# Optimization experiments

Hardware: AMD Instinct MI355X
Metric: run time of the kernel (lower is better)

Reference implementation:

```python
import jax, jax.numpy as jnp
import numpy as np

N = 50000      # nodes
E = 800000     # edges
IN_DIM = 128
HID = 64
OUT = 2


def _sage_conv(h, src, dst, Wl, bl, Wr, n_nodes):
    """PyG SAGEConv (mean aggr): lin_l(mean_{j in N(i)} h_j) + lin_r(h_i).
    Messages flow src -> dst. lin_r has no bias (PyG default)."""
    msg = h[src]                                             # [E, d]
    agg = jax.ops.segment_sum(msg, dst, num_segments=n_nodes)  # [N, d]
    cnt = jax.ops.segment_sum(jnp.ones((msg.shape[0],), h.dtype), dst,
                              num_segments=n_nodes)          # [N]
    agg = agg / jnp.maximum(cnt, 1.0)[:, None]               # mean, zero-deg safe
    return agg @ Wl + bl + h @ Wr


def setup_inputs() -> dict:
    key = jax.random.key(0)
    ks = jax.random.split(key, 12)
    def lin(k, fan_in, fan_out):
        s = 1.0 / np.sqrt(fan_in)
        return jax.random.uniform(k, (fan_in, fan_out), jnp.float32, -s, s)
    x = jax.random.normal(ks[0], (N, IN_DIM), jnp.float32)
    edge_index = jax.random.randint(ks[1], (2, E), 0, N, jnp.int64)
    return {
        "x": x,
        "edge_index": edge_index,
        # conv1
        "W1l": lin(ks[2], IN_DIM, HID),
        "b1l": jnp.zeros((HID,), jnp.float32),
        "W1r": lin(ks[3], IN_DIM, HID),
        # conv2
        "W2l": lin(ks[4], HID, HID),
        "b2l": jnp.zeros((HID,), jnp.float32),
        "W2r": lin(ks[5], HID, HID),
        # edge MLP
        "Wm1": lin(ks[6], 2 * HID, HID),
        "bm1": jnp.zeros((HID,), jnp.float32),
        "Wm2": lin(ks[7], HID, OUT),
        "bm2": jnp.zeros((OUT,), jnp.float32),
    }


def reference(x, edge_index, W1l, b1l, W1r, W2l, b2l, W2r, Wm1, bm1, Wm2, bm2):
    src, dst = edge_index[0], edge_index[1]
    h = jax.nn.relu(_sage_conv(x, src, dst, W1l, b1l, W1r, N))   # [N, HID]
    h = jax.nn.relu(_sage_conv(h, src, dst, W2l, b2l, W2r, N))   # [N, HID]
    edge_rep = jnp.concatenate([h[src], h[dst]], axis=1)          # [E, 2*HID]
    hidden = jax.nn.relu(edge_rep @ Wm1 + bm1)                    # [E, HID]
    return hidden @ Wm2 + bm2                                     # [E, OUT]
```

## Files before the change

kernel.cpp:

```cpp
#include <hip/hip_runtime.h>

#define N_NODES 50000
#define N_EDGES 800000

#define BVALS 64
#define NBUK ((N_NODES + BVALS - 1) / BVALS)
#define PAD 16
#define CHUNK 4096
#define NSB ((N_EDGES + CHUNK - 1) / CHUNK)
#define BCAP 2048
#define PREPB 128

typedef __attribute__((ext_vector_type(8))) short bf16x8;
typedef __attribute__((ext_vector_type(4))) float f32x4;


__device__ __forceinline__ float bf2f(unsigned short u) {
    return __uint_as_float(((unsigned)u) << 16);
}
__device__ __forceinline__ unsigned short f2bf(float f) {
    unsigned u = __float_as_uint(f);
    u += 0x7FFFu + ((u >> 16) & 1u);
    return (unsigned short)(u >> 16);
}
__device__ __forceinline__ unsigned pack2bf(float a, float b) {
    return (unsigned)f2bf(a) | ((unsigned)f2bf(b) << 16);
}
__device__ __forceinline__ float lobf(int w) {
    return __uint_as_float(((unsigned)w) << 16);
}
__device__ __forceinline__ float hibf(int w) {
    return __uint_as_float(((unsigned)w) & 0xFFFF0000u);
}
__device__ __forceinline__ void stv(float* p, float v) { *p = v; }
__device__ __forceinline__ void stv(unsigned short* p, float v) { *p = f2bf(v); }

__device__ __forceinline__ void add8(float* a, int4 v) {
    a[0] += lobf(v.x); a[1] += hibf(v.x);
    a[2] += lobf(v.y); a[3] += hibf(v.y);
    a[4] += lobf(v.z); a[5] += hibf(v.z);
    a[6] += lobf(v.w); a[7] += hibf(v.w);
}


__global__ __launch_bounds__(256) void count_prep_kernel(
        const int* __restrict__ ei, int* __restrict__ bhist,
        const float* __restrict__ W1l, const float* __restrict__ W1r,
        const float* __restrict__ W2l, const float* __restrict__ W2r,
        const float* __restrict__ Wm1,
        unsigned short* __restrict__ wt1, unsigned short* __restrict__ wt2,
        unsigned short* __restrict__ wtm, int E) {
    __shared__ int hist[NBUK];
    int t = threadIdx.x;
    if (blockIdx.x >= NSB) {
        int id = (blockIdx.x - NSB) * 256 + t;
        if (id < 128 * 128) {
            int k = id >> 7, c = id & 127;
            float v = (c < 64) ? W1l[k * 64 + c] : W1r[k * 64 + (c - 64)];
            wt1[c * 128 + k] = f2bf(v);
        } else if (id < 128 * 128 + 64 * 128) {
            int j = id - 128 * 128;
            int k = j >> 7, c = j & 127;
            float v = (c < 64) ? W2l[k * 64 + c] : W2r[k * 64 + (c - 64)];
            wt2[c * 64 + k] = f2bf(v);
        } else if (id < 128 * 128 + 64 * 128 + 64 * 128) {
            int j = id - 128 * 128 - 64 * 128;
            int k = j >> 7, c = j & 127;
            float v = (c < 64) ? Wm1[k * 64 + c] : Wm1[(64 + k) * 64 + (c - 64)];
            wtm[c * 64 + k] = f2bf(v);
        }
        return;
    }
    for (int h = t; h < NBUK; h += 256) hist[h] = 0;
    __syncthreads();
    int e0 = blockIdx.x * CHUNK;
    int ne = min(CHUNK, E - e0);
    for (int i = t; i < ne; i += 256)
        atomicAdd(&hist[ei[E + e0 + i] >> 6], 1);
    __syncthreads();
    for (int h = t; h < NBUK; h += 256)
        bhist[blockIdx.x * NBUK + h] = hist[h];
}

__global__ __launch_bounds__(1024) void scan_bcnt_kernel(
        const int* __restrict__ bhist, int* __restrict__ bofs,
        int* __restrict__ gcur_pad) {
    __shared__ int lds[1024];
    int t = threadIdx.x;
    int v = 0;
    if (t < NBUK)
        for (int b = 0; b < NSB; ++b) v += bhist[b * NBUK + t];
    lds[t] = v;
    __syncthreads();
    for (int off = 1; off < 1024; off <<= 1) {
        int u = (t >= off) ? lds[t - off] : 0;
        __syncthreads();
        lds[t] += u;
        __syncthreads();
    }
    if (t <= NBUK) bofs[t] = lds[t] - ((t < NBUK) ? v : 0);
    if (t < NBUK) gcur_pad[t * PAD] = lds[t] - v;
}

__global__ __launch_bounds__(256) void scatter_kernel(
        const int* __restrict__ ei, int* __restrict__ gcur_pad,
        unsigned int* __restrict__ bpk, int E) {
    __shared__ unsigned int pk[CHUNK];
    __shared__ int hist[NBUK];
    __shared__ int lbase[NBUK];
    int t = threadIdx.x;
    for (int h = t; h < NBUK; h += 256) hist[h] = 0;
    __syncthreads();
    int e0 = blockIdx.x * CHUNK;
    int ne = min(CHUNK, E - e0);
    for (int i = t; i < ne; i += 256) {
        unsigned s = (unsigned)ei[e0 + i];
        unsigned d = (unsigned)ei[E + e0 + i];
        pk[i] = (d << 16) | s;
        atomicAdd(&hist[d >> 6], 1);
    }
    __syncthreads();
    for (int h = t; h < NBUK; h += 256) {
        int c = hist[h];
        lbase[h] = c ? atomicAdd(&gcur_pad[h * PAD], c) : 0;
        hist[h] = 0;
    }
    __syncthreads();
    for (int i = t; i < ne; i += 256) {
        unsigned v = pk[i];
        int h = (v >> 16) >> 6;
        int idx = atomicAdd(&hist[h], 1);
        bpk[lbase[h] + idx] = v;
    }
}


template<int K>
__device__ __forceinline__ void stage_w(
        const unsigned short* __restrict__ WT, unsigned short* w_lds, int t) {
    constexpr int KP = K + 8;
    for (int idx = t; idx < 128 * K / 8; idx += 256) {
        int f = idx * 8;
        int r = f / K, c = f % K;
        *(int4*)&w_lds[r * KP + c] = *(const int4*)&WT[r * K + c];
    }
}

template<int K, typename T0, typename T1>
__device__ __forceinline__ void mfma_tile(
        const unsigned short* a_lds, const unsigned short* w_lds,
        int t, int n0, T0* __restrict__ C0, T1* __restrict__ C1, int N) {
    constexpr int KP = K + 8;
    int w = t >> 6, l = t & 63;
    int lr = l & 15;
    int lk = (l >> 4) * 8;

    f32x4 acc[8];
#pragma unroll
    for (int i = 0; i < 8; ++i) acc[i] = (f32x4)(0.f);

#pragma unroll
    for (int kc = 0; kc < K / 32; ++kc) {
        bf16x8 af = *(const bf16x8*)&a_lds[(w * 16 + lr) * KP + kc * 32 + lk];
#pragma unroll
        for (int ct = 0; ct < 8; ++ct) {
            bf16x8 bfr = *(const bf16x8*)&w_lds[(ct * 16 + lr) * KP + kc * 32 + lk];
            acc[ct] = __builtin_amdgcn_mfma_f32_16x16x32_bf16(af, bfr, acc[ct], 0, 0, 0);
        }
    }

    int orow = n0 + w * 16 + (l >> 4) * 4;
#pragma unroll
    for (int ct = 0; ct < 4; ++ct) {
#pragma unroll
        for (int r = 0; r < 4; ++r) {
            if (orow + r < N) stv(&C0[(size_t)(orow + r) * 64 + ct * 16 + lr], acc[ct][r]);
        }
    }
#pragma unroll
    for (int ct = 4; ct < 8; ++ct) {
#pragma unroll
        for (int r = 0; r < 4; ++r) {
            if (orow + r < N) stv(&C1[(size_t)(orow + r) * 64 + (ct - 4) * 16 + lr], acc[ct][r]);
        }
    }
}


__global__ __launch_bounds__(256) void sort_gemm1_kernel(
        const unsigned int* __restrict__ bpk, const int* __restrict__ bofs,
        int* __restrict__ rowptr, int* __restrict__ elist,
        const float* __restrict__ x, const unsigned short* __restrict__ wt1,
        unsigned short* __restrict__ C0, float* __restrict__ C1, int N) {
    __shared__ __align__(16) char smem[52224];
    int t = threadIdx.x;

    if (blockIdx.x < NBUK) {
        unsigned int* pk = (unsigned int*)smem;
        int* sc  = (int*)(pk + BCAP);
        int* cur = sc + BVALS;
        int b = blockIdx.x;
        int e0 = bofs[b];
        int nb = min(bofs[b + 1] - e0, BCAP);

        if (t < BVALS) sc[t] = 0;
        __syncthreads();
        for (int i = t; i < nb; i += 256) {
            unsigned v = bpk[e0 + i];
            pk[i] = v;
            atomicAdd(&sc[(v >> 16) & 63], 1);
        }
        __syncthreads();
        int hv = (t < BVALS) ? sc[t] : 0;
#pragma unroll
        for (int off = 1; off < BVALS; off <<= 1) {
            int u = (t < BVALS && t >= off) ? sc[t - off] : 0;
            __syncthreads();
            if (t < BVALS) sc[t] += u;
            __syncthreads();
        }
        if (t < BVALS) {
            int ex = sc[t] - hv;
            cur[t] = ex;
            int n = b * BVALS + t;
            if (n <= N) rowptr[n] = e0 + ex;
        }
        __syncthreads();
        for (int i = t; i < nb; i += 256) {
            unsigned v = pk[i];
            int pos = atomicAdd(&cur[(v >> 16) & 63], 1);
            elist[e0 + pos] = v & 0xFFFF;
        }
        return;
    }

    constexpr int K = 128, KP = K + 8;
    unsigned short* a_lds = (unsigned short*)smem;
    unsigned short* w_lds = a_lds + 64 * KP;
    int n0 = (blockIdx.x - NBUK) * 64;

    for (int idx = t; idx < 64 * K / 4; idx += 256) {
        int f = idx * 4;
        int r = f / K, c = f % K;
        float4 v = make_float4(0.f, 0.f, 0.f, 0.f);
        if (n0 + r < N) v = *(const float4*)&x[(size_t)(n0 + r) * K + c];
        ushort4 o;
        o.x = f2bf(v.x); o.y = f2bf(v.y); o.z = f2bf(v.z); o.w = f2bf(v.w);
        *(ushort4*)&a_lds[r * KP + c] = o;
    }
    stage_w<K>(wt1, w_lds, t);
    __syncthreads();
    mfma_tile<K>(a_lds, w_lds, t, n0, C0, C1, N);
}


template<typename T1>
__global__ __launch_bounds__(256) void agg_gemm_kernel(
        const unsigned short* __restrict__ P, const float* __restrict__ R,
        const float* __restrict__ bias,
        const int* __restrict__ rowptr, const int* __restrict__ elist,
        const unsigned short* __restrict__ WT,
        unsigned short* __restrict__ C0, T1* __restrict__ C1, int N) {
    constexpr int K = 64, KP = K + 8;
    __shared__ unsigned short a_lds[64 * KP];
    __shared__ unsigned short w_lds[128 * KP];
    int t = threadIdx.x;
    int n0 = blockIdx.x * 64;

    stage_w<K>(WT, w_lds, t);

    int l8 = t & 7;
    int nr = t >> 3;
    float4 b0 = *(const float4*)&bias[l8 * 8];
    float4 b1 = *(const float4*)&bias[l8 * 8 + 4];

#pragma unroll
    for (int half = 0; half < 2; ++half) {
        int r = half * 32 + nr;
        int n = n0 + r;
        float a0[8] = {0.f, 0.f, 0.f, 0.f, 0.f, 0.f, 0.f, 0.f};
        float a1[8] = {0.f, 0.f, 0.f, 0.f, 0.f, 0.f, 0.f, 0.f};
        int r0 = 0, r1 = 0;
        if (n < N) { r0 = rowptr[n]; r1 = rowptr[n + 1]; }
        int p = r0;
        for (; p + 2 <= r1; p += 2) {
            int sA = elist[p], sB = elist[p + 1];
            int4 vA = *(const int4*)&P[(size_t)sA * 64 + l8 * 8];
            int4 vB = *(const int4*)&P[(size_t)sB * 64 + l8 * 8];
            add8(a0, vA);
            add8(a1, vB);
        }
        if (p < r1) {
            int sA = elist[p];
            add8(a0, *(const int4*)&P[(size_t)sA * 64 + l8 * 8]);
        }
        int4 o = make_int4(0, 0, 0, 0);
        if (n < N) {
            float inv = 1.0f / fmaxf((float)(r1 - r0), 1.0f);
            float4 rA = *(const float4*)&R[(size_t)n * 64 + l8 * 8];
            float4 rB = *(const float4*)&R[(size_t)n * 64 + l8 * 8 + 4];
            float h0 = fmaxf(fmaf(a0[0] + a1[0], inv, b0.x + rA.x), 0.f);
            float h1 = fmaxf(fmaf(a0[1] + a1[1], inv, b0.y + rA.y), 0.f);
            float h2 = fmaxf(fmaf(a0[2] + a1[2], inv, b0.z + rA.z), 0.f);
            float h3 = fmaxf(fmaf(a0[3] + a1[3], inv, b0.w + rA.w), 0.f);
            float h4 = fmaxf(fmaf(a0[4] + a1[4], inv, b1.x + rB.x), 0.f);
            float h5 = fmaxf(fmaf(a0[5] + a1[5], inv, b1.y + rB.y), 0.f);
            float h6 = fmaxf(fmaf(a0[6] + a1[6], inv, b1.z + rB.z), 0.f);
            float h7 = fmaxf(fmaf(a0[7] + a1[7], inv, b1.w + rB.w), 0.f);
            o.x = pack2bf(h0, h1); o.y = pack2bf(h2, h3);
            o.z = pack2bf(h4, h5); o.w = pack2bf(h6, h7);
        }
        *(int4*)&a_lds[r * KP + l8 * 8] = o;
    }
    __syncthreads();
    mfma_tile<K>(a_lds, w_lds, t, n0, C0, C1, N);
}


__global__ __launch_bounds__(256) void edge_out_kernel(
        const unsigned short* __restrict__ Pa, const unsigned short* __restrict__ Pb,
        const int* __restrict__ ei,
        const float* __restrict__ bm1,
        const float* __restrict__ Wm2, const float* __restrict__ bm2,
        float* __restrict__ out, int E) {
    int t = threadIdx.x;
    int l8 = t & 7;
    int eg = t >> 3;
    int base = blockIdx.x * 128 + eg;

    float4 wA = *(const float4*)&Wm2[l8 * 16];
    float4 wB = *(const float4*)&Wm2[l8 * 16 + 4];
    float4 wC = *(const float4*)&Wm2[l8 * 16 + 8];
    float4 wD = *(const float4*)&Wm2[l8 * 16 + 12];
    float4 bbA = *(const float4*)&bm1[l8 * 8];
    float4 bbB = *(const float4*)&bm1[l8 * 8 + 4];
    float ob0 = bm2[0], ob1 = bm2[1];

#pragma unroll
    for (int it = 0; it < 4; ++it) {
        int e = base + it * 32;
        int s = ei[e];
        int d = ei[E + e];
        int4 ua = *(const int4*)&Pa[(size_t)s * 64 + l8 * 8];
        int4 ub = *(const int4*)&Pb[(size_t)d * 64 + l8 * 8];
        float h0 = fmaxf(lobf(ua.x) + lobf(ub.x) + bbA.x, 0.f);
        float h1 = fmaxf(hibf(ua.x) + hibf(ub.x) + bbA.y, 0.f);
        float h2 = fmaxf(lobf(ua.y) + lobf(ub.y) + bbA.z, 0.f);
        float h3 = fmaxf(hibf(ua.y) + hibf(ub.y) + bbA.w, 0.f);
        float h4 = fmaxf(lobf(ua.z) + lobf(ub.z) + bbB.x, 0.f);
        float h5 = fmaxf(hibf(ua.z) + hibf(ub.z) + bbB.y, 0.f);
        float h6 = fmaxf(lobf(ua.w) + lobf(ub.w) + bbB.z, 0.f);
        float h7 = fmaxf(hibf(ua.w) + hibf(ub.w) + bbB.w, 0.f);
        float s0 = h0 * wA.x + h1 * wA.z + h2 * wB.x + h3 * wB.z
                 + h4 * wC.x + h5 * wC.z + h6 * wD.x + h7 * wD.z;
        float s1 = h0 * wA.y + h1 * wA.w + h2 * wB.y + h3 * wB.w
                 + h4 * wC.y + h5 * wC.w + h6 * wD.y + h7 * wD.w;
#pragma unroll
        for (int off = 4; off >= 1; off >>= 1) {
            s0 += __shfl_xor(s0, off, 64);
            s1 += __shfl_xor(s1, off, 64);
        }
        if (l8 == 0) {
            *(float2*)&out[(size_t)e * 2] = make_float2(s0 + ob0, s1 + ob1);
        }
    }
}


extern "C" void kernel_launch(void* const* d_in, const int* in_sizes, int n_in,
                              void* d_out, int out_size, void* d_ws, size_t ws_size,
                              hipStream_t stream) {
    const float* x   = (const float*)d_in[0];
    const int*   ei  = (const int*)d_in[1];
    const float* W1l = (const float*)d_in[2];
    const float* b1l = (const float*)d_in[3];
    const float* W1r = (const float*)d_in[4];
    const float* W2l = (const float*)d_in[5];
    const float* b2l = (const float*)d_in[6];
    const float* W2r = (const float*)d_in[7];
    const float* Wm1 = (const float*)d_in[8];
    const float* bm1 = (const float*)d_in[9];
    const float* Wm2 = (const float*)d_in[10];
    const float* bm2 = (const float*)d_in[11];
    float* out = (float*)d_out;

    const int N = N_NODES, E = N_EDGES;

    float* B0 = (float*)d_ws;
    float* B1 = B0 + (size_t)N * 64;
    float* B2 = B1 + (size_t)N * 64;
    unsigned short* B3h = (unsigned short*)(B2 + (size_t)N * 64);
    int* rowptr   = (int*)(B3h + (size_t)N * 64);
    int* elist    = rowptr + N + 1;
    int* bofs     = elist + E;
    int* gcur_pad = bofs + NBUK + 1;
    int* bhist    = gcur_pad + NBUK * PAD;
    unsigned short* wt1 = (unsigned short*)(bhist + NSB * NBUK);
    unsigned short* wt2 = wt1 + 128 * 128;
    unsigned short* wtm = wt2 + 128 * 64;
    unsigned int* bpk = (unsigned int*)B2;

    unsigned short* B0h = (unsigned short*)B0;
    unsigned short* B2h = (unsigned short*)B2;

    count_prep_kernel<<<NSB + PREPB, 256, 0, stream>>>(
        ei, bhist, W1l, W1r, W2l, W2r, Wm1, wt1, wt2, wtm, E);
    scan_bcnt_kernel<<<1, 1024, 0, stream>>>(bhist, bofs, gcur_pad);
    scatter_kernel<<<NSB, 256, 0, stream>>>(ei, gcur_pad, bpk, E);

    sort_gemm1_kernel<<<NBUK + (N + 63) / 64, 256, 0, stream>>>(
        bpk, bofs, rowptr, elist, x, wt1, B0h, B1, N);

    agg_gemm_kernel<float><<<(N + 63) / 64, 256, 0, stream>>>(
        B0h, B1, b1l, rowptr, elist, wt2, B2h, B1, N);

    agg_gemm_kernel<unsigned short><<<(N + 63) / 64, 256, 0, stream>>>(
        B2h, B1, b2l, rowptr, elist, wtm, B0h, B3h, N);

    edge_out_kernel<<<E / 128, 256, 0, stream>>>(B0h, B3h, ei, bm1, Wm2, bm2, out, E);
}
```

Measured before the change: 142.2 us.

## Process edge MLP per destination node via CSR and store root term in bf16

The sort now carries each edge's original index, so the edge-output kernel can walk the CSR per destination node. It loads the destination projection and bias once per node and scatters results to the original edge positions. It also stores the lin_r/root intermediate as bf16 instead of fp32 and unrolls the aggregation loop to four accumulators. Costs: the sort traffic doubles (uint2 entries), an extra eidx array is written and read, output writes become scattered, and load balance depends on node degree.

After: 165.5 us, median of 2. 1.16x slower.

```diff
diff --git a/kernel.cpp b/kernel.cpp
--- a/kernel.cpp
+++ b/kernel.cpp
@@ -102,10 +102,11 @@
     if (t < NBUK) gcur_pad[t * PAD] = lds[t] - v;
 }
 
+
 __global__ __launch_bounds__(256) void scatter_kernel(
         const int* __restrict__ ei, int* __restrict__ gcur_pad,
-        unsigned int* __restrict__ bpk, int E) {
-    __shared__ unsigned int pk[CHUNK];
+        uint2* __restrict__ bpk, int E) {
+    __shared__ uint2 pk[CHUNK];
     __shared__ int hist[NBUK];
     __shared__ int lbase[NBUK];
     int t = threadIdx.x;
@@ -116,7 +117,7 @@
     for (int i = t; i < ne; i += 256) {
         unsigned s = (unsigned)ei[e0 + i];
         unsigned d = (unsigned)ei[E + e0 + i];
-        pk[i] = (d << 16) | s;
+        pk[i] = make_uint2((d << 16) | s, (unsigned)(e0 + i));
         atomicAdd(&hist[d >> 6], 1);
     }
     __syncthreads();
@@ -127,8 +128,8 @@
     }
     __syncthreads();
     for (int i = t; i < ne; i += 256) {
-        unsigned v = pk[i];
-        int h = (v >> 16) >> 6;
+        uint2 v = pk[i];
+        int h = (v.x >> 16) >> 6;
         int idx = atomicAdd(&hist[h], 1);
         bpk[lbase[h] + idx] = v;
     }
@@ -188,15 +189,15 @@
 
 
 __global__ __launch_bounds__(256) void sort_gemm1_kernel(
-        const unsigned int* __restrict__ bpk, const int* __restrict__ bofs,
-        int* __restrict__ rowptr, int* __restrict__ elist,
+        const uint2* __restrict__ bpk, const int* __restrict__ bofs,
+        int* __restrict__ rowptr, int* __restrict__ elist, int* __restrict__ eidx,
         const float* __restrict__ x, const unsigned short* __restrict__ wt1,
-        unsigned short* __restrict__ C0, float* __restrict__ C1, int N) {
+        unsigned short* __restrict__ C0, unsigned short* __restrict__ C1, int N) {
     __shared__ __align__(16) char smem[52224];
     int t = threadIdx.x;
 
     if (blockIdx.x < NBUK) {
-        unsigned int* pk = (unsigned int*)smem;
+        uint2* pk = (uint2*)smem;
         int* sc  = (int*)(pk + BCAP);
         int* cur = sc + BVALS;
         int b = blockIdx.x;
@@ -206,9 +207,9 @@
         if (t < BVALS) sc[t] = 0;
         __syncthreads();
         for (int i = t; i < nb; i += 256) {
-            unsigned v = bpk[e0 + i];
+            uint2 v = bpk[e0 + i];
             pk[i] = v;
-            atomicAdd(&sc[(v >> 16) & 63], 1);
+            atomicAdd(&sc[(v.x >> 16) & 63], 1);
         }
         __syncthreads();
         int hv = (t < BVALS) ? sc[t] : 0;
@@ -227,9 +228,10 @@
         }
         __syncthreads();
         for (int i = t; i < nb; i += 256) {
-            unsigned v = pk[i];
-            int pos = atomicAdd(&cur[(v >> 16) & 63], 1);
-            elist[e0 + pos] = v & 0xFFFF;
+            uint2 v = pk[i];
+            int pos = e0 + atomicAdd(&cur[(v.x >> 16) & 63], 1);
+            elist[pos] = v.x & 0xFFFF;
+            eidx[pos] = (int)v.y;
         }
         return;
     }
@@ -254,13 +256,12 @@
 }
 
 
-template<typename T1>
 __global__ __launch_bounds__(256) void agg_gemm_kernel(
-        const unsigned short* __restrict__ P, const float* __restrict__ R,
+        const unsigned short* __restrict__ P, const unsigned short* __restrict__ R,
         const float* __restrict__ bias,
         const int* __restrict__ rowptr, const int* __restrict__ elist,
         const unsigned short* __restrict__ WT,
-        unsigned short* __restrict__ C0, T1* __restrict__ C1, int N) {
+        unsigned short* __restrict__ C0, unsigned short* __restrict__ C1, int N) {
     constexpr int K = 64, KP = K + 8;
     __shared__ unsigned short a_lds[64 * KP];
     __shared__ unsigned short w_lds[128 * KP];
@@ -280,33 +281,36 @@
         int n = n0 + r;
         float a0[8] = {0.f, 0.f, 0.f, 0.f, 0.f, 0.f, 0.f, 0.f};
         float a1[8] = {0.f, 0.f, 0.f, 0.f, 0.f, 0.f, 0.f, 0.f};
+        float a2[8] = {0.f, 0.f, 0.f, 0.f, 0.f, 0.f, 0.f, 0.f};
+        float a3[8] = {0.f, 0.f, 0.f, 0.f, 0.f, 0.f, 0.f, 0.f};
         int r0 = 0, r1 = 0;
         if (n < N) { r0 = rowptr[n]; r1 = rowptr[n + 1]; }
         int p = r0;
-        for (; p + 2 <= r1; p += 2) {
-            int sA = elist[p], sB = elist[p + 1];
+        for (; p + 4 <= r1; p += 4) {
+            int sA = elist[p],     sB = elist[p + 1];
+            int sC = elist[p + 2], sD = elist[p + 3];
             int4 vA = *(const int4*)&P[(size_t)sA * 64 + l8 * 8];
             int4 vB = *(const int4*)&P[(size_t)sB * 64 + l8 * 8];
-            add8(a0, vA);
-            add8(a1, vB);
-        }
-        if (p < r1) {
+            int4 vC = *(const int4*)&P[(size_t)sC * 64 + l8 * 8];
+            int4 vD = *(const int4*)&P[(size_t)sD * 64 + l8 * 8];
+            add8(a0, vA); add8(a1, vB); add8(a2, vC); add8(a3, vD);
+        }
+        for (; p < r1; ++p) {
             int sA = elist[p];
             add8(a0, *(const int4*)&P[(size_t)sA * 64 + l8 * 8]);
         }
         int4 o = make_int4(0, 0, 0, 0);
         if (n < N) {
             float inv = 1.0f / fmaxf((float)(r1 - r0), 1.0f);
-            float4 rA = *(const float4*)&R[(size_t)n * 64 + l8 * 8];
-            float4 rB = *(const float4*)&R[(size_t)n * 64 + l8 * 8 + 4];
-            float h0 = fmaxf(fmaf(a0[0] + a1[0], inv, b0.x + rA.x), 0.f);
-            float h1 = fmaxf(fmaf(a0[1] + a1[1], inv, b0.y + rA.y), 0.f);
-            float h2 = fmaxf(fmaf(a0[2] + a1[2], inv, b0.z + rA.z), 0.f);
-            float h3 = fmaxf(fmaf(a0[3] + a1[3], inv, b0.w + rA.w), 0.f);
-            float h4 = fmaxf(fmaf(a0[4] + a1[4], inv, b1.x + rB.x), 0.f);
-            float h5 = fmaxf(fmaf(a0[5] + a1[5], inv, b1.y + rB.y), 0.f);
-            float h6 = fmaxf(fmaf(a0[6] + a1[6], inv, b1.z + rB.z), 0.f);
-            float h7 = fmaxf(fmaf(a0[7] + a1[7], inv, b1.w + rB.w), 0.f);
+            int4 rv = *(const int4*)&R[(size_t)n * 64 + l8 * 8];
+            float h0 = fmaxf(fmaf(a0[0] + a1[0] + a2[0] + a3[0], inv, b0.x + lobf(rv.x)), 0.f);
+            float h1 = fmaxf(fmaf(a0[1] + a1[1] + a2[1] + a3[1], inv, b0.y + hibf(rv.x)), 0.f);
+            float h2 = fmaxf(fmaf(a0[2] + a1[2] + a2[2] + a3[2], inv, b0.z + lobf(rv.y)), 0.f);
+            float h3 = fmaxf(fmaf(a0[3] + a1[3] + a2[3] + a3[3], inv, b0.w + hibf(rv.y)), 0.f);
+            float h4 = fmaxf(fmaf(a0[4] + a1[4] + a2[4] + a3[4], inv, b1.x + lobf(rv.z)), 0.f);
+            float h5 = fmaxf(fmaf(a0[5] + a1[5] + a2[5] + a3[5], inv, b1.y + hibf(rv.z)), 0.f);
+            float h6 = fmaxf(fmaf(a0[6] + a1[6] + a2[6] + a3[6], inv, b1.z + lobf(rv.w)), 0.f);
+            float h7 = fmaxf(fmaf(a0[7] + a1[7] + a2[7] + a3[7], inv, b1.w + hibf(rv.w)), 0.f);
             o.x = pack2bf(h0, h1); o.y = pack2bf(h2, h3);
             o.z = pack2bf(h4, h5); o.w = pack2bf(h6, h7);
         }
@@ -319,14 +323,15 @@
 
 __global__ __launch_bounds__(256) void edge_out_kernel(
         const unsigned short* __restrict__ Pa, const unsigned short* __restrict__ Pb,
-        const int* __restrict__ ei,
+        const int* __restrict__ rowptr, const int* __restrict__ elist,
+        const int* __restrict__ eidx,
         const float* __restrict__ bm1,
         const float* __restrict__ Wm2, const float* __restrict__ bm2,
-        float* __restrict__ out, int E) {
+        float* __restrict__ out, int N) {
     int t = threadIdx.x;
     int l8 = t & 7;
-    int eg = t >> 3;
-    int base = blockIdx.x * 128 + eg;
+    int n = blockIdx.x * 32 + (t >> 3);
+    if (n >= N) return;
 
     float4 wA = *(const float4*)&Wm2[l8 * 16];
     float4 wB = *(const float4*)&Wm2[l8 * 16 + 4];
@@ -336,21 +341,57 @@
     float4 bbB = *(const float4*)&bm1[l8 * 8 + 4];
     float ob0 = bm2[0], ob1 = bm2[1];
 
-#pragma unroll
-    for (int it = 0; it < 4; ++it) {
-        int e = base + it * 32;
-        int s = ei[e];
-        int d = ei[E + e];
-        int4 ua = *(const int4*)&Pa[(size_t)s * 64 + l8 * 8];
-        int4 ub = *(const int4*)&Pb[(size_t)d * 64 + l8 * 8];
-        float h0 = fmaxf(lobf(ua.x) + lobf(ub.x) + bbA.x, 0.f);
-        float h1 = fmaxf(hibf(ua.x) + hibf(ub.x) + bbA.y, 0.f);
-        float h2 = fmaxf(lobf(ua.y) + lobf(ub.y) + bbA.z, 0.f);
-        float h3 = fmaxf(hibf(ua.y) + hibf(ub.y) + bbA.w, 0.f);
-        float h4 = fmaxf(lobf(ua.z) + lobf(ub.z) + bbB.x, 0.f);
-        float h5 = fmaxf(hibf(ua.z) + hibf(ub.z) + bbB.y, 0.f);
-        float h6 = fmaxf(lobf(ua.w) + lobf(ub.w) + bbB.z, 0.f);
-        float h7 = fmaxf(hibf(ua.w) + hibf(ub.w) + bbB.w, 0.f);
+    int4 vb = *(const int4*)&Pb[(size_t)n * 64 + l8 * 8];
+    float q0 = lobf(vb.x) + bbA.x, q1 = hibf(vb.x) + bbA.y;
+    float q2 = lobf(vb.y) + bbA.z, q3 = hibf(vb.y) + bbA.w;
+    float q4 = lobf(vb.z) + bbB.x, q5 = hibf(vb.z) + bbB.y;
+    float q6 = lobf(vb.w) + bbB.z, q7 = hibf(vb.w) + bbB.w;
+
+    int r0 = rowptr[n], r1 = rowptr[n + 1];
+    int p = r0;
+    for (; p + 2 <= r1; p += 2) {
+        int sA = elist[p], sB = elist[p + 1];
+        int4 ua = *(const int4*)&Pa[(size_t)sA * 64 + l8 * 8];
+        int4 ub = *(const int4*)&Pa[(size_t)sB * 64 + l8 * 8];
+        float h0 = fmaxf(lobf(ua.x) + q0, 0.f), g0 = fmaxf(lobf(ub.x) + q0, 0.f);
+        float h1 = fmaxf(hibf(ua.x) + q1, 0.f), g1 = fmaxf(hibf(ub.x) + q1, 0.f);
+        float h2 = fmaxf(lobf(ua.y) + q2, 0.f), g2 = fmaxf(lobf(ub.y) + q2, 0.f);
+        float h3 = fmaxf(hibf(ua.y) + q3, 0.f), g3 = fmaxf(hibf(ub.y) + q3, 0.f);
+        float h4 = fmaxf(lobf(ua.z) + q4, 0.f), g4 = fmaxf(lobf(ub.z) + q4, 0.f);
+        float h5 = fmaxf(hibf(ua.z) + q5, 0.f), g5 = fmaxf(hibf(ub.z) + q5, 0.f);
+        float h6 = fmaxf(lobf(ua.w) + q6, 0.f), g6 = fmaxf(lobf(ub.w) + q6, 0.f);
+        float h7 = fmaxf(hibf(ua.w) + q7, 0.f), g7 = fmaxf(hibf(ub.w) + q7, 0.f);
+        float sa0 = h0 * wA.x + h1 * wA.z + h2 * wB.x + h3 * wB.z
+                  + h4 * wC.x + h5 * wC.z + h6 * wD.x + h7 * wD.z;
+        float sa1 = h0 * wA.y + h1 * wA.w + h2 * wB.y + h3 * wB.w
+                  + h4 * wC.y + h5 * wC.w + h6 * wD.y + h7 * wD.w;
+        float sb0 = g0 * wA.x + g1 * wA.z + g2 * wB.x + g3 * wB.z
+                  + g4 * wC.x + g5 * wC.z + g6 * wD.x + g7 * wD.z;
+        float sb1 = g0 * wA.y + g1 * wA.w + g2 * wB.y + g3 * wB.w
+                  + g4 * wC.y + g5 * wC.w + g6 * wD.y + g7 * wD.w;
+#pragma unroll
+        for (int off = 4; off >= 1; off >>= 1) {
+            sa0 += __shfl_xor(sa0, off, 64);
+            sa1 += __shfl_xor(sa1, off, 64);
+            sb0 += __shfl_xor(sb0, off, 64);
+            sb1 += __shfl_xor(sb1, off, 64);
+        }
+        if (l8 == 0) {
+            *(float2*)&out[(size_t)eidx[p] * 2]     = make_float2(sa0 + ob0, sa1 + ob1);
+            *(float2*)&out[(size_t)eidx[p + 1] * 2] = make_float2(sb0 + ob0, sb1 + ob1);
+        }
+    }
+    if (p < r1) {
+        int sA = elist[p];
+        int4 ua = *(const int4*)&Pa[(size_t)sA * 64 + l8 * 8];
+        float h0 = fmaxf(lobf(ua.x) + q0, 0.f);
+        float h1 = fmaxf(hibf(ua.x) + q1, 0.f);
+        float h2 = fmaxf(lobf(ua.y) + q2, 0.f);
+        float h3 = fmaxf(hibf(ua.y) + q3, 0.f);
+        float h4 = fmaxf(lobf(ua.z) + q4, 0.f);
+        float h5 = fmaxf(hibf(ua.z) + q5, 0.f);
+        float h6 = fmaxf(lobf(ua.w) + q6, 0.f);
+        float h7 = fmaxf(hibf(ua.w) + q7, 0.f);
         float s0 = h0 * wA.x + h1 * wA.z + h2 * wB.x + h3 * wB.z
                  + h4 * wC.x + h5 * wC.z + h6 * wD.x + h7 * wD.z;
         float s1 = h0 * wA.y + h1 * wA.w + h2 * wB.y + h3 * wB.w
@@ -361,7 +402,7 @@
             s1 += __shfl_xor(s1, off, 64);
         }
         if (l8 == 0) {
-            *(float2*)&out[(size_t)e * 2] = make_float2(s0 + ob0, s1 + ob1);
+            *(float2*)&out[(size_t)eidx[p] * 2] = make_float2(s0 + ob0, s1 + ob1);
         }
     }
 }
@@ -392,15 +433,17 @@
     unsigned short* B3h = (unsigned short*)(B2 + (size_t)N * 64);
     int* rowptr   = (int*)(B3h + (size_t)N * 64);
     int* elist    = rowptr + N + 1;
-    int* bofs     = elist + E;
+    int* eidx     = elist + E;
+    int* bofs     = eidx + E;
     int* gcur_pad = bofs + NBUK + 1;
     int* bhist    = gcur_pad + NBUK * PAD;
     unsigned short* wt1 = (unsigned short*)(bhist + NSB * NBUK);
     unsigned short* wt2 = wt1 + 128 * 128;
     unsigned short* wtm = wt2 + 128 * 64;
-    unsigned int* bpk = (unsigned int*)B2;
+    uint2* bpk = (uint2*)B2;
 
     unsigned short* B0h = (unsigned short*)B0;
+    unsigned short* B1h = (unsigned short*)B1;
     unsigned short* B2h = (unsigned short*)B2;
 
     count_prep_kernel<<<NSB + PREPB, 256, 0, stream>>>(
@@ -409,13 +452,14 @@
     scatter_kernel<<<NSB, 256, 0, stream>>>(ei, gcur_pad, bpk, E);
 
     sort_gemm1_kernel<<<NBUK + (N + 63) / 64, 256, 0, stream>>>(
-        bpk, bofs, rowptr, elist, x, wt1, B0h, B1, N);
-
-    agg_gemm_kernel<float><<<(N + 63) / 64, 256, 0, stream>>>(
-        B0h, B1, b1l, rowptr, elist, wt2, B2h, B1, N);
-
-    agg_gemm_kernel<unsigned short><<<(N + 63) / 64, 256, 0, stream>>>(
-        B2h, B1, b2l, rowptr, elist, wtm, B0h, B3h, N);
-
-    edge_out_kernel<<<E / 128, 256, 0, stream>>>(B0h, B3h, ei, bm1, Wm2, bm2, out, E);
-}
+        bpk, bofs, rowptr, elist, eidx, x, wt1, B0h, B1h, N);
+
+    agg_gemm_kernel<<<(N + 63) / 64, 256, 0, stream>>>(
+        B0h, B1h, b1l, rowptr, elist, wt2, B2h, B1h, N);
+
+    agg_gemm_kernel<<<(N + 63) / 64, 256, 0, stream>>>(
+        B2h, B1h, b2l, rowptr, elist, wtm, B0h, B3h, N);
+
+    edge_out_kernel<<<(N + 31) / 32, 256, 0, stream>>>(
+        B0h, B3h, rowptr, elist, eidx, bm1, Wm2, bm2, out, N);
+}
```
